# Performance work log

Measured on AMD Instinct MI355X. Metric: run time of the kernel, lower is better.

## Reference

```python
import jax, jax.numpy as jnp
import numpy as np

DIM = 1024
HEADS = 16


def setup_inputs() -> dict:
    key = jax.random.key(0)
    k1, k2, k3, k4 = jax.random.split(key, 4)
    x = jax.random.normal(k1, (4, 2048, DIM), dtype=jnp.float32)
    s = 1.0 / np.sqrt(DIM)
    w_qkv = jax.random.normal(k2, (DIM, 3 * DIM), dtype=jnp.float32) * s
    w_out = jax.random.normal(k3, (DIM, DIM), dtype=jnp.float32) * s
    b_out = jax.random.normal(k4, (DIM,), dtype=jnp.float32) * 0.01
    return {"x": x, "w_qkv": w_qkv, "w_out": w_out, "b_out": b_out}


def reference(x, w_qkv, w_out, b_out):
    b, n, d = x.shape
    h = HEADS
    dh = d // h
    scale = dh ** -0.5
    qkv = x @ w_qkv  # [b, n, 3d]
    q, k, v = jnp.split(qkv, 3, axis=-1)
    # [b, n, d] -> [b, h, n, dh]
    def to_heads(t):
        return t.reshape(b, n, h, dh).transpose(0, 2, 1, 3)
    q, k, v = to_heads(q), to_heads(k), to_heads(v)
    dots = jnp.einsum('bhid,bhjd->bhij', q, k) * scale
    attn = jax.nn.softmax(dots, axis=-1)
    out = jnp.einsum('bhij,bhjd->bhid', attn, v)
    out = out.transpose(0, 2, 1, 3).reshape(b, n, d)
    return out @ w_out + b_out
```

## Files before the change

### kernel.cpp

```cpp
#include <hip/hip_runtime.h>
#include <hip/hip_bf16.h>


typedef __attribute__((ext_vector_type(4))) float f32x4;
typedef __attribute__((ext_vector_type(16))) float f32x16;
typedef __attribute__((ext_vector_type(8))) unsigned short u16x8;
typedef __attribute__((ext_vector_type(4))) unsigned short u16x4;
typedef __attribute__((ext_vector_type(4))) unsigned int u32x4;
typedef __attribute__((ext_vector_type(8))) __bf16 bf16x8;

static __device__ __forceinline__ f32x4 mfma_bf16(u16x8 a, u16x8 b, f32x4 c) {
    return __builtin_amdgcn_mfma_f32_16x16x32_bf16(
        __builtin_bit_cast(bf16x8, a), __builtin_bit_cast(bf16x8, b), c, 0, 0, 0);
}
static __device__ __forceinline__ f32x16 mfma32(u16x8 a, u16x8 b, f32x16 c) {
    return __builtin_amdgcn_mfma_f32_32x32x16_bf16(
        __builtin_bit_cast(bf16x8, a), __builtin_bit_cast(bf16x8, b), c, 0, 0, 0);
}

static __device__ __forceinline__ unsigned short f2bf(float f) {
    unsigned int u = __builtin_bit_cast(unsigned int, f);
    u += 0x7fffu + ((u >> 16) & 1u);
    return (unsigned short)(u >> 16);
}
static __device__ __forceinline__ unsigned int cvt_pk_bf16(float a, float b) {
    unsigned int r;
    asm("v_cvt_pk_bf16_f32 %0, %1, %2" : "=v"(r) : "v"(a), "v"(b));
    return r;
}
static __device__ __forceinline__ float fexp2(float x) {
    float r;
    asm("v_exp_f32 %0, %1" : "=v"(r) : "v"(x));
    return r;
}
static __device__ __forceinline__ float frcp(float x) {
    float r;
    asm("v_rcp_f32 %0, %1" : "=v"(r) : "v"(x));
    return r;
}
typedef const __attribute__((address_space(1))) unsigned int* gp1_t;
typedef __attribute__((address_space(3))) unsigned int* lp3_t;
static __device__ __forceinline__ void gl_lds16(const void* g, void* l) {
    __builtin_amdgcn_global_load_lds((gp1_t)g, (lp3_t)l, 16, 0, 0);
}

__global__ void k_cvt(const float* __restrict__ in, unsigned short* __restrict__ out, int n4) {
    int i = blockIdx.x * blockDim.x + threadIdx.x;
    int stride = gridDim.x * blockDim.x;
    for (; i < n4; i += stride) {
        f32x4 v = ((const f32x4*)in)[i];
        u16x4 o;
        #pragma unroll
        for (int j = 0; j < 4; ++j) o[j] = f2bf(v[j]);
        ((u16x4*)out)[i] = o;
    }
}

__global__ void k_transpose_sc(const float* __restrict__ in, unsigned short* __restrict__ out,
                               int R, int C, int scale_rows, float scale) {
    __shared__ float tile[32][33];
    int c0 = blockIdx.x * 32, r0 = blockIdx.y * 32;
    int tx = threadIdx.x, ty = threadIdx.y;
    #pragma unroll
    for (int i = ty; i < 32; i += 8)
        tile[i][tx] = in[(size_t)(r0 + i) * C + c0 + tx];
    __syncthreads();
    #pragma unroll
    for (int i = ty; i < 32; i += 8) {
        float v = tile[tx][i];
        if (c0 + i < scale_rows) v *= scale;
        out[(size_t)(c0 + i) * R + r0 + tx] = f2bf(v);
    }
}

__global__ __launch_bounds__(512, 1) void k_gemm1(
    const unsigned short* __restrict__ A,
    const unsigned short* __restrict__ BT,
    unsigned short* __restrict__ qkv)
{
    __shared__ unsigned short As[3][256 * 64];
    __shared__ unsigned short Bs[3][128 * 64];
    const int K = 1024;
    const int tid = threadIdx.x, lane = tid & 63, wave = tid >> 6;

    int lin = blockIdx.y * 24 + blockIdx.x;
    int xcd = lin & 7, idx = lin >> 3;
    int chunk = idx / 12, c = idx % 12;
    int by = xcd * 4 + (c / 3);
    int bx = chunk * 3 + (c % 3);
    const int m0 = by * 256, n0 = bx * 128;

    const int wm = (wave >> 1) * 64, wn = (wave & 1) * 64;
    const int lr = lane & 15, half = lane >> 4;
    const int srow = lane >> 3, sslot = lane & 7;

    auto stage_sub = [&](int buf, int t, int h) {
        int k0 = t * 64;
        #pragma unroll
        for (int r = 0; r < 2; ++r) {
            int chunkc = (h * 2 + r) * 8 + wave;
            int row = chunkc * 8 + srow;
            int koff = (sslot ^ (row & 7)) * 8;
            gl_lds16(&A[(size_t)(m0 + row) * K + k0 + koff], &As[buf][chunkc * 512]);
        }
        {
            int chunkc = h * 8 + wave;
            int row = chunkc * 8 + srow;
            int koff = (sslot ^ (row & 7)) * 8;
            gl_lds16(&BT[(size_t)(n0 + row) * K + k0 + koff], &Bs[buf][chunkc * 512]);
        }
    };

    f32x4 acc[4][4] = {};

    stage_sub(0, 0, 0); stage_sub(0, 0, 1);
    stage_sub(1, 1, 0); stage_sub(1, 1, 1);
    asm volatile("s_waitcnt vmcnt(6)" ::: "memory");
    __builtin_amdgcn_s_barrier();

    for (int t = 0; t < 16; ++t) {
        const int cur = t % 3, nxt = (t + 2) % 3;
        const bool do_stage = (t + 2) < 16;
        const unsigned short* Ab = As[cur];
        const unsigned short* Bb = Bs[cur];

        #pragma unroll
        for (int ks = 0; ks < 2; ++ks) {
            u16x8 af[4], bfr[4];
            #pragma unroll
            for (int i = 0; i < 4; ++i) {
                int ra = wm + i * 16 + lr;
                af[i] = *(const u16x8*)&Ab[ra * 64 + (((ks * 4 + half) ^ (ra & 7)) * 8)];
                int rb = wn + i * 16 + lr;
                bfr[i] = *(const u16x8*)&Bb[rb * 64 + (((ks * 4 + half) ^ (rb & 7)) * 8)];
            }
            if (do_stage) stage_sub(nxt, t + 2, ks);
            if (ks == 1) {
                if (t < 14)       asm volatile("s_waitcnt vmcnt(6)" ::: "memory");
                else if (t == 14) asm volatile("s_waitcnt vmcnt(0)" ::: "memory");
            }
            __builtin_amdgcn_s_barrier();
            asm volatile("s_waitcnt lgkmcnt(0)" ::: "memory");
            __builtin_amdgcn_sched_barrier(0);
            __builtin_amdgcn_s_setprio(1);
            #pragma unroll
            for (int i = 0; i < 4; ++i)
                #pragma unroll
                for (int j = 0; j < 4; ++j)
                    acc[i][j] = mfma_bf16(af[i], bfr[j], acc[i][j]);
            __builtin_amdgcn_s_setprio(0);
            __builtin_amdgcn_s_barrier();
        }
    }

    #pragma unroll
    for (int i = 0; i < 4; ++i)
        #pragma unroll
        for (int j = 0; j < 4; ++j)
            #pragma unroll
            for (int r = 0; r < 4; ++r) {
                int row = m0 + wm + i * 16 + half * 4 + r;
                int col = n0 + wn + j * 16 + lr;
                qkv[(size_t)row * 3072 + col] = f2bf(acc[i][j][r]);
            }
}

__global__ void k_vtrans(const unsigned short* __restrict__ qkv,
                         unsigned short* __restrict__ VTs) {
    __shared__ unsigned short tile[32][33];
    int bh = blockIdx.y >> 1, dt = blockIdx.y & 1;
    int b = bh >> 4, h = bh & 15;
    int n0 = blockIdx.x * 32, d0 = dt * 32;
    int tx = threadIdx.x, ty = threadIdx.y;
    const unsigned short* src = qkv + (size_t)(b * 2048) * 3072 + 2048 + h * 64 + d0;
    #pragma unroll
    for (int i = ty; i < 32; i += 8)
        tile[i][tx] = src[(size_t)(n0 + i) * 3072 + tx];
    __syncthreads();
    #pragma unroll
    for (int i = ty; i < 32; i += 8)
        VTs[((size_t)bh * 64 + d0 + i) * 2048 + n0 + tx] = tile[tx][i];
}

__global__ __launch_bounds__(512, 1) void k_gemm2(
    const unsigned short* __restrict__ A,
    const unsigned short* __restrict__ BT,
    const float* __restrict__ bias,
    float* __restrict__ outf)
{
    __shared__ unsigned short As[3][256 * 64];
    __shared__ unsigned short Bs[3][128 * 64];
    const int K = 1024;
    const int tid = threadIdx.x, lane = tid & 63, wave = tid >> 6;

    int gx = gridDim.x;
    int nwg = gx * gridDim.y;
    int lin = blockIdx.y * gx + blockIdx.x;
    int virt = (lin & 7) * (nwg >> 3) + (lin >> 3);
    int bx = virt % gx, by = virt / gx;
    const int m0 = by * 256, n0 = bx * 128;

    const int wm = (wave >> 1) * 64, wn = (wave & 1) * 64;
    const int lr = lane & 15, half = lane >> 4;
    const int srow = lane >> 3, sslot = lane & 7;

    auto stage_sub = [&](int buf, int t, int h) {
        int k0 = t * 64;
        #pragma unroll
        for (int r = 0; r < 2; ++r) {
            int chunk = (h * 2 + r) * 8 + wave;
            int row = chunk * 8 + srow;
            int koff = (sslot ^ (row & 7)) * 8;
            gl_lds16(&A[(size_t)(m0 + row) * K + k0 + koff], &As[buf][chunk * 512]);
        }
        {
            int chunk = h * 8 + wave;
            int row = chunk * 8 + srow;
            int koff = (sslot ^ (row & 7)) * 8;
            gl_lds16(&BT[(size_t)(n0 + row) * K + k0 + koff], &Bs[buf][chunk * 512]);
        }
    };

    f32x4 acc[4][4] = {};

    stage_sub(0, 0, 0); stage_sub(0, 0, 1);
    stage_sub(1, 1, 0); stage_sub(1, 1, 1);
    asm volatile("s_waitcnt vmcnt(6)" ::: "memory");
    __builtin_amdgcn_s_barrier();

    for (int t = 0; t < 16; ++t) {
        const int cur = t % 3, nxt = (t + 2) % 3;
        const bool do_stage = (t + 2) < 16;
        const unsigned short* Ab = As[cur];
        const unsigned short* Bb = Bs[cur];

        #pragma unroll
        for (int ks = 0; ks < 2; ++ks) {
            u16x8 af[4], bfr[4];
            #pragma unroll
            for (int i = 0; i < 4; ++i) {
                int ra = wm + i * 16 + lr;
                af[i] = *(const u16x8*)&Ab[ra * 64 + (((ks * 4 + half) ^ (ra & 7)) * 8)];
                int rb = wn + i * 16 + lr;
                bfr[i] = *(const u16x8*)&Bb[rb * 64 + (((ks * 4 + half) ^ (rb & 7)) * 8)];
            }
            if (do_stage) stage_sub(nxt, t + 2, ks);
            if (ks == 1) {
                if (t < 14)       asm volatile("s_waitcnt vmcnt(6)" ::: "memory");
                else if (t == 14) asm volatile("s_waitcnt vmcnt(0)" ::: "memory");
            }
            __builtin_amdgcn_s_barrier();
            asm volatile("s_waitcnt lgkmcnt(0)" ::: "memory");
            __builtin_amdgcn_sched_barrier(0);
            __builtin_amdgcn_s_setprio(1);
            #pragma unroll
            for (int i = 0; i < 4; ++i)
                #pragma unroll
                for (int j = 0; j < 4; ++j)
                    acc[i][j] = mfma_bf16(af[i], bfr[j], acc[i][j]);
            __builtin_amdgcn_s_setprio(0);
            __builtin_amdgcn_s_barrier();
        }
    }

    #pragma unroll
    for (int i = 0; i < 4; ++i)
        #pragma unroll
        for (int j = 0; j < 4; ++j)
            #pragma unroll
            for (int r = 0; r < 4; ++r) {
                int row = m0 + wm + i * 16 + half * 4 + r;
                int col = n0 + wn + j * 16 + lr;
                outf[(size_t)row * 1024 + col] = acc[i][j][r] + bias[col];
            }
}

__global__ __launch_bounds__(256, 4) void k_attn(
    const unsigned short* __restrict__ qkv,
    const unsigned short* __restrict__ VTs,
    unsigned short* __restrict__ attn)
{
    __shared__ unsigned short Kt[2][64 * 64];
    __shared__ unsigned short Vt[2][64 * 64];
    const int tid = threadIdx.x, lane = tid & 63, wave = tid >> 6;

    int lin = blockIdx.y * 16 + blockIdx.x;
    int virt = (lin & 7) * 128 + (lin >> 3);
    int bh = virt >> 4;
    int q0 = (virt & 15) * 128 + wave * 32;

    const int lq = lane & 31;
    const int hi = lane >> 5;

    int b = bh >> 4, h = bh & 15;
    const unsigned short* Kq = qkv + (size_t)(b * 2048) * 3072 + 1024 + h * 64;
    const unsigned short* Vbase = VTs + (size_t)bh * 64 * 2048;

    u16x8 qf[4];
    {
        const unsigned short* Qr = qkv + (size_t)(b * 2048 + q0 + lq) * 3072 + h * 64;
        #pragma unroll
        for (int kk = 0; kk < 4; ++kk)
            qf[kk] = *(const u16x8*)&Qr[kk * 16 + hi * 8];
    }

    const int srow_in = lane >> 4, sslot = lane & 15;
    auto stage = [&](int buf, int j0) {
        #pragma unroll
        for (int c = 0; c < 2; ++c) {
            int chunk = wave * 2 + c;
            int row = chunk * 4 + srow_in;
            int v = sslot ^ (row & 15);
            int high = v >> 3, dsl = (v & 7) * 8;
            gl_lds16(Kq + (size_t)(j0 + high * 32 + row) * 3072 + dsl, &Kt[buf][chunk * 512]);
            gl_lds16(Vbase + (size_t)(high * 32 + row) * 2048 + j0 + dsl, &Vt[buf][chunk * 512]);
        }
    };

    f32x16 o[2] = {};
    f32x16 osum = {};
    const u16x8 onesf = {0x3F80, 0x3F80, 0x3F80, 0x3F80, 0x3F80, 0x3F80, 0x3F80, 0x3F80};

    stage(0, 0);
    __syncthreads();
    int cur = 0;

    for (int t = 0; t < 32; ++t) {
        if (t < 31) stage(cur ^ 1, (t + 1) * 64);

        f32x16 sacc[2] = {};
        __builtin_amdgcn_s_setprio(1);
        #pragma unroll
        for (int jb = 0; jb < 2; ++jb) {
            u16x8 kf[4];
            #pragma unroll
            for (int kk = 0; kk < 4; ++kk) {
                int s = (jb * 8 + kk * 2 + hi) ^ (lq & 15);
                kf[kk] = *(const u16x8*)&Kt[cur][lq * 128 + s * 8];
            }
            #pragma unroll
            for (int kk = 0; kk < 4; ++kk)
                sacc[jb] = mfma32(kf[kk], qf[kk], sacc[jb]);
        }
        __builtin_amdgcn_s_setprio(0);

        unsigned int pk[16];
        #pragma unroll
        for (int jb = 0; jb < 2; ++jb)
            #pragma unroll
            for (int i = 0; i < 8; ++i)
                pk[jb * 8 + i] = cvt_pk_bf16(fexp2(sacc[jb][2 * i]), fexp2(sacc[jb][2 * i + 1]));

        __builtin_amdgcn_s_setprio(1);
        #pragma unroll
        for (int kk = 0; kk < 4; ++kk) {
            const int base = (kk >> 1) * 8 + (kk & 1) * 4;
            unsigned int w0 = pk[base + 0], w2 = pk[base + 2];
            unsigned int w1 = pk[base + 1], w3 = pk[base + 3];
            asm("v_permlane32_swap_b32 %0, %1" : "+v"(w0), "+v"(w2));
            asm("v_permlane32_swap_b32 %0, %1" : "+v"(w1), "+v"(w3));
            u32x4 w; w[0] = w0; w[1] = w1; w[2] = w2; w[3] = w3;
            u16x8 pa = __builtin_bit_cast(u16x8, w);
            osum = mfma32(pa, onesf, osum);
            #pragma unroll
            for (int db = 0; db < 2; ++db) {
                int s = (db * 8 + kk * 2 + hi) ^ (lq & 15);
                u16x8 vf = *(const u16x8*)&Vt[cur][lq * 128 + s * 8];
                o[db] = mfma32(pa, vf, o[db]);
            }
        }
        __builtin_amdgcn_s_setprio(0);

        __syncthreads();
        cur ^= 1;
    }

    #pragma unroll
    for (int r = 0; r < 16; ++r) {
        int qrow = (r & 3) + 8 * (r >> 2) + 4 * hi;
        float invr = frcp(osum[r]);
        size_t ro = (size_t)(b * 2048 + q0 + qrow) * 1024 + h * 64;
        attn[ro + lq]      = f2bf(o[0][r] * invr);
        attn[ro + 32 + lq] = f2bf(o[1][r] * invr);
    }
}

extern "C" void kernel_launch(void* const* d_in, const int* in_sizes, int n_in,
                              void* d_out, int out_size, void* d_ws, size_t ws_size,
                              hipStream_t stream) {
    const float* x     = (const float*)d_in[0];
    const float* w_qkv = (const float*)d_in[1];
    const float* w_out = (const float*)d_in[2];
    const float* b_out = (const float*)d_in[3];
    float* out = (float*)d_out;

    char* ws = (char*)d_ws;
    size_t off = 0;
    auto alloc = [&](size_t bytes) -> void* {
        void* p = ws + off;
        off += (bytes + 255) & ~(size_t)255;
        return p;
    };
    unsigned short* xb    = (unsigned short*)alloc(8192ull * 1024 * 2);
    unsigned short* wqkvT = (unsigned short*)alloc(3072ull * 1024 * 2);
    unsigned short* woutT = (unsigned short*)alloc(1024ull * 1024 * 2);
    unsigned short* qkv   = (unsigned short*)alloc(8192ull * 3072 * 2);
    unsigned short* VTs   = (unsigned short*)alloc(64ull * 2048 * 64 * 2);
    if (off > ws_size) return;

    k_cvt<<<2048, 256, 0, stream>>>(x, xb, 8192 * 1024 / 4);
    k_transpose_sc<<<dim3(3072 / 32, 1024 / 32), dim3(32, 8), 0, stream>>>(
        w_qkv, wqkvT, 1024, 3072, 1024, 0.18033688f);
    k_transpose_sc<<<dim3(1024 / 32, 1024 / 32), dim3(32, 8), 0, stream>>>(
        w_out, woutT, 1024, 1024, 0, 1.0f);
    k_gemm1<<<dim3(24, 32), 512, 0, stream>>>(xb, wqkvT, qkv);
    k_vtrans<<<dim3(64, 128), dim3(32, 8), 0, stream>>>(qkv, VTs);
    k_attn<<<dim3(16, 64), 256, 0, stream>>>(qkv, VTs, xb);
    k_gemm2<<<dim3(8, 32), 512, 0, stream>>>(xb, woutT, b_out, out);
}
```

Before: 194.0 us.

## Split fused QKV projection into three separate GEMMs writing contiguous Q, K, V

The single 768-workgroup QKV GEMM is replaced by three 256-workgroup launches of a generic GEMM. Each launch writes its own 1024-wide Q, K or V buffer, so attention and the V transpose read rows with a 1024 stride instead of 3072. The intent is denser memory access downstream. The cost is two extra kernel launches, three rereads of the activation matrix, and 256-block grids that may fill the GPU less evenly than the fused 768-block grid.

```diff
diff --git a/kernel.cpp b/kernel.cpp
--- a/kernel.cpp
+++ b/kernel.cpp
@@ -73,21 +73,19 @@
     }
 }
 
-__global__ __launch_bounds__(512, 1) void k_gemm1(
+__global__ __launch_bounds__(512, 1) void k_gemmb(
     const unsigned short* __restrict__ A,
     const unsigned short* __restrict__ BT,
-    unsigned short* __restrict__ qkv)
+    unsigned short* __restrict__ O)
 {
     __shared__ unsigned short As[3][256 * 64];
     __shared__ unsigned short Bs[3][128 * 64];
     const int K = 1024;
     const int tid = threadIdx.x, lane = tid & 63, wave = tid >> 6;
 
-    int lin = blockIdx.y * 24 + blockIdx.x;
-    int xcd = lin & 7, idx = lin >> 3;
-    int chunk = idx / 12, c = idx % 12;
-    int by = xcd * 4 + (c / 3);
-    int bx = chunk * 3 + (c % 3);
+    int lin = blockIdx.y * 8 + blockIdx.x;
+    int virt = (lin & 7) * 32 + (lin >> 3);
+    int bx = virt % 8, by = virt / 8;
     const int m0 = by * 256, n0 = bx * 128;
 
     const int wm = (wave >> 1) * 64, wn = (wave & 1) * 64;
@@ -98,16 +96,16 @@
         int k0 = t * 64;
         #pragma unroll
         for (int r = 0; r < 2; ++r) {
-            int chunkc = (h * 2 + r) * 8 + wave;
-            int row = chunkc * 8 + srow;
+            int chunk = (h * 2 + r) * 8 + wave;
+            int row = chunk * 8 + srow;
             int koff = (sslot ^ (row & 7)) * 8;
-            gl_lds16(&A[(size_t)(m0 + row) * K + k0 + koff], &As[buf][chunkc * 512]);
+            gl_lds16(&A[(size_t)(m0 + row) * K + k0 + koff], &As[buf][chunk * 512]);
         }
         {
-            int chunkc = h * 8 + wave;
-            int row = chunkc * 8 + srow;
+            int chunk = h * 8 + wave;
+            int row = chunk * 8 + srow;
             int koff = (sslot ^ (row & 7)) * 8;
-            gl_lds16(&BT[(size_t)(n0 + row) * K + k0 + koff], &Bs[buf][chunkc * 512]);
+            gl_lds16(&BT[(size_t)(n0 + row) * K + k0 + koff], &Bs[buf][chunk * 512]);
         }
     };
 
@@ -161,21 +159,21 @@
             for (int r = 0; r < 4; ++r) {
                 int row = m0 + wm + i * 16 + half * 4 + r;
                 int col = n0 + wn + j * 16 + lr;
-                qkv[(size_t)row * 3072 + col] = f2bf(acc[i][j][r]);
-            }
-}
-
-__global__ void k_vtrans(const unsigned short* __restrict__ qkv,
+                O[(size_t)row * 1024 + col] = f2bf(acc[i][j][r]);
+            }
+}
+
+__global__ void k_vtrans(const unsigned short* __restrict__ Vb,
                          unsigned short* __restrict__ VTs) {
     __shared__ unsigned short tile[32][33];
     int bh = blockIdx.y >> 1, dt = blockIdx.y & 1;
     int b = bh >> 4, h = bh & 15;
     int n0 = blockIdx.x * 32, d0 = dt * 32;
     int tx = threadIdx.x, ty = threadIdx.y;
-    const unsigned short* src = qkv + (size_t)(b * 2048) * 3072 + 2048 + h * 64 + d0;
+    const unsigned short* src = Vb + (size_t)(b * 2048) * 1024 + h * 64 + d0;
     #pragma unroll
     for (int i = ty; i < 32; i += 8)
-        tile[i][tx] = src[(size_t)(n0 + i) * 3072 + tx];
+        tile[i][tx] = src[(size_t)(n0 + i) * 1024 + tx];
     __syncthreads();
     #pragma unroll
     for (int i = ty; i < 32; i += 8)
@@ -193,11 +191,9 @@
     const int K = 1024;
     const int tid = threadIdx.x, lane = tid & 63, wave = tid >> 6;
 
-    int gx = gridDim.x;
-    int nwg = gx * gridDim.y;
-    int lin = blockIdx.y * gx + blockIdx.x;
-    int virt = (lin & 7) * (nwg >> 3) + (lin >> 3);
-    int bx = virt % gx, by = virt / gx;
+    int lin = blockIdx.y * 8 + blockIdx.x;
+    int virt = (lin & 7) * 32 + (lin >> 3);
+    int bx = virt % 8, by = virt / 8;
     const int m0 = by * 256, n0 = bx * 128;
 
     const int wm = (wave >> 1) * 64, wn = (wave & 1) * 64;
@@ -276,7 +272,8 @@
 }
 
 __global__ __launch_bounds__(256, 4) void k_attn(
-    const unsigned short* __restrict__ qkv,
+    const unsigned short* __restrict__ Qb,
+    const unsigned short* __restrict__ Kb,
     const unsigned short* __restrict__ VTs,
     unsigned short* __restrict__ attn)
 {
@@ -293,12 +290,12 @@
     const int hi = lane >> 5;
 
     int b = bh >> 4, h = bh & 15;
-    const unsigned short* Kq = qkv + (size_t)(b * 2048) * 3072 + 1024 + h * 64;
+    const unsigned short* Kq = Kb + (size_t)(b * 2048) * 1024 + h * 64;
     const unsigned short* Vbase = VTs + (size_t)bh * 64 * 2048;
 
     u16x8 qf[4];
     {
-        const unsigned short* Qr = qkv + (size_t)(b * 2048 + q0 + lq) * 3072 + h * 64;
+        const unsigned short* Qr = Qb + (size_t)(b * 2048 + q0 + lq) * 1024 + h * 64;
         #pragma unroll
         for (int kk = 0; kk < 4; ++kk)
             qf[kk] = *(const u16x8*)&Qr[kk * 16 + hi * 8];
@@ -312,7 +309,7 @@
             int row = chunk * 4 + srow_in;
             int v = sslot ^ (row & 15);
             int high = v >> 3, dsl = (v & 7) * 8;
-            gl_lds16(Kq + (size_t)(j0 + high * 32 + row) * 3072 + dsl, &Kt[buf][chunk * 512]);
+            gl_lds16(Kq + (size_t)(j0 + high * 32 + row) * 1024 + dsl, &Kt[buf][chunk * 512]);
             gl_lds16(Vbase + (size_t)(high * 32 + row) * 2048 + j0 + dsl, &Vt[buf][chunk * 512]);
         }
     };
@@ -404,7 +401,9 @@
     unsigned short* xb    = (unsigned short*)alloc(8192ull * 1024 * 2);
     unsigned short* wqkvT = (unsigned short*)alloc(3072ull * 1024 * 2);
     unsigned short* woutT = (unsigned short*)alloc(1024ull * 1024 * 2);
-    unsigned short* qkv   = (unsigned short*)alloc(8192ull * 3072 * 2);
+    unsigned short* Qb    = (unsigned short*)alloc(8192ull * 1024 * 2);
+    unsigned short* Kb    = (unsigned short*)alloc(8192ull * 1024 * 2);
+    unsigned short* Vb    = (unsigned short*)alloc(8192ull * 1024 * 2);
     unsigned short* VTs   = (unsigned short*)alloc(64ull * 2048 * 64 * 2);
     if (off > ws_size) return;
 
@@ -413,8 +412,10 @@
         w_qkv, wqkvT, 1024, 3072, 1024, 0.18033688f);
     k_transpose_sc<<<dim3(1024 / 32, 1024 / 32), dim3(32, 8), 0, stream>>>(
         w_out, woutT, 1024, 1024, 0, 1.0f);
-    k_gemm1<<<dim3(24, 32), 512, 0, stream>>>(xb, wqkvT, qkv);
-    k_vtrans<<<dim3(64, 128), dim3(32, 8), 0, stream>>>(qkv, VTs);
-    k_attn<<<dim3(16, 64), 256, 0, stream>>>(qkv, VTs, xb);
+    k_gemmb<<<dim3(8, 32), 512, 0, stream>>>(xb, wqkvT,                Qb);
+    k_gemmb<<<dim3(8, 32), 512, 0, stream>>>(xb, wqkvT + 1024 * 1024,  Kb);
+    k_gemmb<<<dim3(8, 32), 512, 0, stream>>>(xb, wqkvT + 2048 * 1024,  Vb);
+    k_vtrans<<<dim3(64, 128), dim3(32, 8), 0, stream>>>(Vb, VTs);
+    k_attn<<<dim3(16, 64), 256, 0, stream>>>(Qb, Kb, VTs, xb);
     k_gemm2<<<dim3(8, 32), 512, 0, stream>>>(xb, woutT, b_out, out);
 }
```

After: 201.7 us. 1.04x slower.

## Make QKV GEMM persistent over three N tiles per workgroup

Applied to the files above, without the earlier changes.

The QKV projection GEMM now launches 256 workgroups, one per CU, instead of 768. Each workgroup walks three N tiles in sequence inside a single 48-step pipelined K loop, storing and zeroing its accumulators after every 16 steps. This removes the partial-wave tail from 768 tiles on 256 CUs and keeps the load pipeline running across tile boundaries. The cost is a serialized epilogue store in the middle of the loop, plus a different L2 locality pattern because the XCD swizzle was changed. The gemm2 swizzle is also hardcoded to its grid size.

```diff
diff --git a/kernel.cpp b/kernel.cpp
--- a/kernel.cpp
+++ b/kernel.cpp
@@ -73,7 +73,7 @@
     }
 }
 
-__global__ __launch_bounds__(512, 1) void k_gemm1(
+__global__ __launch_bounds__(512, 1) void k_gemm1p(
     const unsigned short* __restrict__ A,
     const unsigned short* __restrict__ BT,
     unsigned short* __restrict__ qkv)
@@ -83,31 +83,30 @@
     const int K = 1024;
     const int tid = threadIdx.x, lane = tid & 63, wave = tid >> 6;
 
-    int lin = blockIdx.y * 24 + blockIdx.x;
-    int xcd = lin & 7, idx = lin >> 3;
-    int chunk = idx / 12, c = idx % 12;
-    int by = xcd * 4 + (c / 3);
-    int bx = chunk * 3 + (c % 3);
-    const int m0 = by * 256, n0 = bx * 128;
+    int lin = blockIdx.y * 8 + blockIdx.x;
+    int virt = (lin & 7) * 32 + (lin >> 3);
+    int bxg = virt % 8, by = virt / 8;
+    const int m0 = by * 256;
 
     const int wm = (wave >> 1) * 64, wn = (wave & 1) * 64;
     const int lr = lane & 15, half = lane >> 4;
     const int srow = lane >> 3, sslot = lane & 7;
 
-    auto stage_sub = [&](int buf, int t, int h) {
-        int k0 = t * 64;
+    auto stage_sub = [&](int buf, int g, int h) {
+        int k0 = (g & 15) * 64;
+        int n0 = ((g >> 4) * 8 + bxg) * 128;
         #pragma unroll
         for (int r = 0; r < 2; ++r) {
-            int chunkc = (h * 2 + r) * 8 + wave;
-            int row = chunkc * 8 + srow;
+            int chunk = (h * 2 + r) * 8 + wave;
+            int row = chunk * 8 + srow;
             int koff = (sslot ^ (row & 7)) * 8;
-            gl_lds16(&A[(size_t)(m0 + row) * K + k0 + koff], &As[buf][chunkc * 512]);
+            gl_lds16(&A[(size_t)(m0 + row) * K + k0 + koff], &As[buf][chunk * 512]);
         }
         {
-            int chunkc = h * 8 + wave;
-            int row = chunkc * 8 + srow;
+            int chunk = h * 8 + wave;
+            int row = chunk * 8 + srow;
             int koff = (sslot ^ (row & 7)) * 8;
-            gl_lds16(&BT[(size_t)(n0 + row) * K + k0 + koff], &Bs[buf][chunkc * 512]);
+            gl_lds16(&BT[(size_t)(n0 + row) * K + k0 + koff], &Bs[buf][chunk * 512]);
         }
     };
 
@@ -118,9 +117,9 @@
     asm volatile("s_waitcnt vmcnt(6)" ::: "memory");
     __builtin_amdgcn_s_barrier();
 
-    for (int t = 0; t < 16; ++t) {
+    for (int t = 0; t < 48; ++t) {
         const int cur = t % 3, nxt = (t + 2) % 3;
-        const bool do_stage = (t + 2) < 16;
+        const bool do_stage = (t + 2) < 48;
         const unsigned short* Ab = As[cur];
         const unsigned short* Bb = Bs[cur];
 
@@ -136,8 +135,8 @@
             }
             if (do_stage) stage_sub(nxt, t + 2, ks);
             if (ks == 1) {
-                if (t < 14)       asm volatile("s_waitcnt vmcnt(6)" ::: "memory");
-                else if (t == 14) asm volatile("s_waitcnt vmcnt(0)" ::: "memory");
+                if (t < 46)       asm volatile("s_waitcnt vmcnt(6)" ::: "memory");
+                else if (t == 46) asm volatile("s_waitcnt vmcnt(0)" ::: "memory");
             }
             __builtin_amdgcn_s_barrier();
             asm volatile("s_waitcnt lgkmcnt(0)" ::: "memory");
@@ -151,18 +150,23 @@
             __builtin_amdgcn_s_setprio(0);
             __builtin_amdgcn_s_barrier();
         }
-    }
-
-    #pragma unroll
-    for (int i = 0; i < 4; ++i)
-        #pragma unroll
-        for (int j = 0; j < 4; ++j)
-            #pragma unroll
-            for (int r = 0; r < 4; ++r) {
-                int row = m0 + wm + i * 16 + half * 4 + r;
-                int col = n0 + wn + j * 16 + lr;
-                qkv[(size_t)row * 3072 + col] = f2bf(acc[i][j][r]);
-            }
+
+        if ((t & 15) == 15) {
+            int n0 = ((t >> 4) * 8 + bxg) * 128;
+            #pragma unroll
+            for (int i = 0; i < 4; ++i)
+                #pragma unroll
+                for (int j = 0; j < 4; ++j) {
+                    #pragma unroll
+                    for (int r = 0; r < 4; ++r) {
+                        int row = m0 + wm + i * 16 + half * 4 + r;
+                        int col = n0 + wn + j * 16 + lr;
+                        qkv[(size_t)row * 3072 + col] = f2bf(acc[i][j][r]);
+                    }
+                    acc[i][j] = f32x4{0.f, 0.f, 0.f, 0.f};
+                }
+        }
+    }
 }
 
 __global__ void k_vtrans(const unsigned short* __restrict__ qkv,
@@ -193,11 +197,9 @@
     const int K = 1024;
     const int tid = threadIdx.x, lane = tid & 63, wave = tid >> 6;
 
-    int gx = gridDim.x;
-    int nwg = gx * gridDim.y;
-    int lin = blockIdx.y * gx + blockIdx.x;
-    int virt = (lin & 7) * (nwg >> 3) + (lin >> 3);
-    int bx = virt % gx, by = virt / gx;
+    int lin = blockIdx.y * 8 + blockIdx.x;
+    int virt = (lin & 7) * 32 + (lin >> 3);
+    int bx = virt % 8, by = virt / 8;
     const int m0 = by * 256, n0 = bx * 128;
 
     const int wm = (wave >> 1) * 64, wn = (wave & 1) * 64;
@@ -413,7 +415,7 @@
         w_qkv, wqkvT, 1024, 3072, 1024, 0.18033688f);
     k_transpose_sc<<<dim3(1024 / 32, 1024 / 32), dim3(32, 8), 0, stream>>>(
         w_out, woutT, 1024, 1024, 0, 1.0f);
-    k_gemm1<<<dim3(24, 32), 512, 0, stream>>>(xb, wqkvT, qkv);
+    k_gemm1p<<<dim3(8, 32), 512, 0, stream>>>(xb, wqkvT, qkv);
     k_vtrans<<<dim3(64, 128), dim3(32, 8), 0, stream>>>(qkv, VTs);
     k_attn<<<dim3(16, 64), 256, 0, stream>>>(qkv, VTs, xb);
     k_gemm2<<<dim3(8, 32), 512, 0, stream>>>(xb, woutT, b_out, out);
```

Measured after the change: 193.3 us. Within noise of the previous version (-0.4%).
